# Performance work log

Hardware: AMD Instinct MI355X
Metric: run time of the kernel (lower is better)

## Reference

```python
import jax, jax.numpy as jnp
import numpy as np

N_NODES = 50000
N_EDGES = 600000
D_FEAT = 128
HIDDEN = 128
OUT = 64


def sage_conv(x, src, dst, Wl, bl, Wr, n_nodes):
    # message = x[src] gathered per edge; mean-aggregated at dst
    msg = x[src]                                            # [E, d]
    agg = jax.ops.segment_sum(msg, dst, num_segments=n_nodes)   # [N, d]
    cnt = jax.ops.segment_sum(jnp.ones((src.shape[0],), x.dtype), dst,
                              num_segments=n_nodes)             # [N]
    mean = agg / jnp.maximum(cnt, 1.0)[:, None]
    # PyG SAGEConv: lin_l(mean_neighbors) + lin_r(x_root); only lin_l has bias
    return mean @ Wl + bl + x @ Wr


def setup_inputs() -> dict:
    key = jax.random.key(0)
    ks = jax.random.split(key, 7)
    x = jax.random.normal(ks[0], (N_NODES, D_FEAT), dtype=jnp.float32)
    edge_index = jax.random.randint(ks[1], (2, N_EDGES), 0, N_NODES, dtype=jnp.int64)
    s1 = 1.0 / np.sqrt(D_FEAT)
    s2 = 1.0 / np.sqrt(HIDDEN)
    W1l = jax.random.normal(ks[2], (D_FEAT, HIDDEN), dtype=jnp.float32) * s1
    b1l = jnp.zeros((HIDDEN,), dtype=jnp.float32)
    W1r = jax.random.normal(ks[3], (D_FEAT, HIDDEN), dtype=jnp.float32) * s1
    W2l = jax.random.normal(ks[4], (HIDDEN, OUT), dtype=jnp.float32) * s2
    b2l = jnp.zeros((OUT,), dtype=jnp.float32)
    W2r = jax.random.normal(ks[5], (HIDDEN, OUT), dtype=jnp.float32) * s2
    return {"x": x, "edge_index": edge_index, "W1l": W1l, "b1l": b1l,
            "W1r": W1r, "W2l": W2l, "b2l": b2l, "W2r": W2r}


def reference(x, edge_index, W1l, b1l, W1r, W2l, b2l, W2r):
    n = x.shape[0]
    src, dst = edge_index[0], edge_index[1]
    h = sage_conv(x, src, dst, W1l, b1l, W1r, n)
    h = jax.nn.relu(h)
    out = sage_conv(h, src, dst, W2l, b2l, W2r, n)
    return out
```

## Files before the change

### kernel.cpp

```cpp
#include <hip/hip_runtime.h>
#include <cstdint>
#include <cstddef>

#define D 128
#define O2 64
#define PAD 136
#define CAP 64

typedef __attribute__((ext_vector_type(8))) short bf16x8;
typedef __attribute__((ext_vector_type(4))) float f32x4;

__device__ inline unsigned short f2bf(float f) {
  union { float f; uint32_t u; } v; v.f = f;
  uint32_t r = v.u + 0x7FFF + ((v.u >> 16) & 1);
  return (unsigned short)(r >> 16);
}
__device__ inline float bf_lo(uint32_t w) {
  union { uint32_t u; float f; } v; v.u = w << 16; return v.f;
}
__device__ inline float bf_hi(uint32_t w) {
  union { uint32_t u; float f; } v; v.u = w & 0xFFFF0000u; return v.f;
}

__global__ __launch_bounds__(256) void prep_edges(
    const int* __restrict__ src, const int* __restrict__ dst,
    int* __restrict__ deg, unsigned short* __restrict__ eidx, int n_edges)
{
  const int half = n_edges >> 1;
  int e = blockIdx.x * 256 + threadIdx.x;
  if (e < half) {
    int d0 = dst[e],        d1 = dst[e + half];
    int s0 = src[e],        s1 = src[e + half];
    int p0 = atomicAdd(&deg[d0], 1);
    int p1 = atomicAdd(&deg[d1], 1);
    if (p0 < CAP)
      __builtin_nontemporal_store((unsigned short)s0, eidx + (size_t)d0 * CAP + p0);
    if (p1 < CAP)
      __builtin_nontemporal_store((unsigned short)s1, eidx + (size_t)d1 * CAP + p1);
  }
}

__global__ __launch_bounds__(256) void prep_xw(
    const float* __restrict__ x, const float* __restrict__ W1l,
    const float* __restrict__ W1r, const float* __restrict__ W2l,
    const float* __restrict__ W2r, unsigned short* __restrict__ xb,
    unsigned short* __restrict__ WT1, unsigned short* __restrict__ WT2,
    int n_nodes, int xb_blocks)
{
  int b = blockIdx.x;
  if (b < xb_blocks) {
    int i = b * 256 + threadIdx.x;
    if (i < n_nodes * 32) {
      int n = i >> 5, q = i & 31;
      float4 v = ((const float4*)x)[(size_t)n * 32 + q];
      unsigned long long o =
          (unsigned long long)f2bf(v.x)
        | ((unsigned long long)f2bf(v.y) << 16)
        | ((unsigned long long)f2bf(v.z) << 32)
        | ((unsigned long long)f2bf(v.w) << 48);
      __builtin_nontemporal_store(o, (unsigned long long*)(xb + (size_t)n * 128 + q * 4));
    }
  } else {
    int t = (b - xb_blocks) * 256 + threadIdx.x;
    if (t < 128 * 256) {
      int n = t >> 8, k = t & 255;
      float w = (k < 128) ? W1l[(size_t)k * 128 + n] : W1r[(size_t)(k - 128) * 128 + n];
      WT1[t] = f2bf(w);
    } else {
      int u = t - 128 * 256;
      if (u < 128 * 128) {
        int n = u >> 7, k = u & 127;
        float w = (n < 64) ? W2l[(size_t)k * 64 + n] : W2r[(size_t)k * 64 + (n - 64)];
        WT2[u] = f2bf(w);
      }
    }
  }
}

__global__ __launch_bounds__(256) void gather1_kernel(
    const unsigned short* __restrict__ xb, const unsigned short* __restrict__ eidx,
    const int* __restrict__ deg, unsigned short* __restrict__ mean, int n_nodes)
{
  const int j = threadIdx.x & 7;
  const int g = threadIdx.x >> 3;
  const int n = blockIdx.x * 32 + g;
  if (n >= n_nodes) return;
  const int dg = deg[n];
  const int cnt = min(dg, CAP);
  const unsigned short* bucket = eidx + (size_t)n * CAP;
  float a[16];
  #pragma unroll
  for (int i = 0; i < 16; i++) a[i] = 0.f;
  int p = 0;
  for (; p + 8 <= cnt; p += 8) {
    uint4 bi = *(const uint4*)(bucket + p);
    int s[8];
    s[0] = bi.x & 0xFFFF; s[1] = bi.x >> 16;
    s[2] = bi.y & 0xFFFF; s[3] = bi.y >> 16;
    s[4] = bi.z & 0xFFFF; s[5] = bi.z >> 16;
    s[6] = bi.w & 0xFFFF; s[7] = bi.w >> 16;
    uint4 v0[8], v1[8];
    #pragma unroll
    for (int q = 0; q < 8; q++) {
      const unsigned short* r = xb + (size_t)s[q] * 128 + j * 16;
      v0[q] = *(const uint4*)r;
      v1[q] = *(const uint4*)(r + 8);
    }
    #pragma unroll
    for (int q = 0; q < 8; q++) {
      a[0]+=bf_lo(v0[q].x); a[1]+=bf_hi(v0[q].x);
      a[2]+=bf_lo(v0[q].y); a[3]+=bf_hi(v0[q].y);
      a[4]+=bf_lo(v0[q].z); a[5]+=bf_hi(v0[q].z);
      a[6]+=bf_lo(v0[q].w); a[7]+=bf_hi(v0[q].w);
      a[8]+=bf_lo(v1[q].x); a[9]+=bf_hi(v1[q].x);
      a[10]+=bf_lo(v1[q].y); a[11]+=bf_hi(v1[q].y);
      a[12]+=bf_lo(v1[q].z); a[13]+=bf_hi(v1[q].z);
      a[14]+=bf_lo(v1[q].w); a[15]+=bf_hi(v1[q].w);
    }
  }
  for (; p + 4 <= cnt; p += 4) {
    uint2 bi = *(const uint2*)(bucket + p);
    int s[4];
    s[0] = bi.x & 0xFFFF; s[1] = bi.x >> 16;
    s[2] = bi.y & 0xFFFF; s[3] = bi.y >> 16;
    uint4 v0[4], v1[4];
    #pragma unroll
    for (int q = 0; q < 4; q++) {
      const unsigned short* r = xb + (size_t)s[q] * 128 + j * 16;
      v0[q] = *(const uint4*)r;
      v1[q] = *(const uint4*)(r + 8);
    }
    #pragma unroll
    for (int q = 0; q < 4; q++) {
      a[0]+=bf_lo(v0[q].x); a[1]+=bf_hi(v0[q].x);
      a[2]+=bf_lo(v0[q].y); a[3]+=bf_hi(v0[q].y);
      a[4]+=bf_lo(v0[q].z); a[5]+=bf_hi(v0[q].z);
      a[6]+=bf_lo(v0[q].w); a[7]+=bf_hi(v0[q].w);
      a[8]+=bf_lo(v1[q].x); a[9]+=bf_hi(v1[q].x);
      a[10]+=bf_lo(v1[q].y); a[11]+=bf_hi(v1[q].y);
      a[12]+=bf_lo(v1[q].z); a[13]+=bf_hi(v1[q].z);
      a[14]+=bf_lo(v1[q].w); a[15]+=bf_hi(v1[q].w);
    }
  }
  for (; p < cnt; p++) {
    const unsigned short* rA = xb + (size_t)bucket[p] * 128 + j * 16;
    uint4 vA0 = *(const uint4*)rA, vA1 = *(const uint4*)(rA + 8);
    a[0]+=bf_lo(vA0.x); a[1]+=bf_hi(vA0.x); a[2]+=bf_lo(vA0.y); a[3]+=bf_hi(vA0.y);
    a[4]+=bf_lo(vA0.z); a[5]+=bf_hi(vA0.z); a[6]+=bf_lo(vA0.w); a[7]+=bf_hi(vA0.w);
    a[8]+=bf_lo(vA1.x); a[9]+=bf_hi(vA1.x); a[10]+=bf_lo(vA1.y); a[11]+=bf_hi(vA1.y);
    a[12]+=bf_lo(vA1.z); a[13]+=bf_hi(vA1.z); a[14]+=bf_lo(vA1.w); a[15]+=bf_hi(vA1.w);
  }
  const float ic = 1.0f / fmaxf((float)dg, 1.0f);
  uint4 o0, o1;
  o0.x = ((uint32_t)f2bf(a[1]*ic) << 16) | f2bf(a[0]*ic);
  o0.y = ((uint32_t)f2bf(a[3]*ic) << 16) | f2bf(a[2]*ic);
  o0.z = ((uint32_t)f2bf(a[5]*ic) << 16) | f2bf(a[4]*ic);
  o0.w = ((uint32_t)f2bf(a[7]*ic) << 16) | f2bf(a[6]*ic);
  o1.x = ((uint32_t)f2bf(a[9]*ic) << 16) | f2bf(a[8]*ic);
  o1.y = ((uint32_t)f2bf(a[11]*ic) << 16) | f2bf(a[10]*ic);
  o1.z = ((uint32_t)f2bf(a[13]*ic) << 16) | f2bf(a[12]*ic);
  o1.w = ((uint32_t)f2bf(a[15]*ic) << 16) | f2bf(a[14]*ic);
  unsigned short* mr = mean + (size_t)n * 128 + j * 16;
  *(uint4*)mr = o0;
  *(uint4*)(mr + 8) = o1;
}

__global__ __launch_bounds__(64, 2) void l12_mfma(
    const unsigned short* __restrict__ mean, const unsigned short* __restrict__ xb,
    const unsigned short* __restrict__ WT1, const unsigned short* __restrict__ WT2,
    const float* __restrict__ b1l, unsigned short* __restrict__ hl,
    float* __restrict__ outp, int n_nodes)
{
  __shared__ unsigned short s_h[32 * PAD];
  const int lane = threadIdx.x;
  const int quad = lane >> 4, l15 = lane & 15;
  const int N0 = blockIdx.x * 32;
  const int ra0 = min(N0 + l15, n_nodes - 1);
  const int ra1 = min(N0 + 16 + l15, n_nodes - 1);

  bf16x8 af[2][8];
  #pragma unroll
  for (int s = 0; s < 4; s++) {
    af[0][s]     = *(const bf16x8*)(mean + (size_t)ra0 * 128 + quad * 8 + s * 32);
    af[1][s]     = *(const bf16x8*)(mean + (size_t)ra1 * 128 + quad * 8 + s * 32);
    af[0][s + 4] = *(const bf16x8*)(xb   + (size_t)ra0 * 128 + quad * 8 + s * 32);
    af[1][s + 4] = *(const bf16x8*)(xb   + (size_t)ra1 * 128 + quad * 8 + s * 32);
  }

  f32x4 acc[2][8];
  #pragma unroll
  for (int rt = 0; rt < 2; rt++)
    #pragma unroll
    for (int tt = 0; tt < 8; tt++) acc[rt][tt] = (f32x4){0.f, 0.f, 0.f, 0.f};

  const unsigned short* b1 = WT1 + (size_t)l15 * 256 + quad * 8;
  bf16x8 cur[8], nxt[8];
  #pragma unroll
  for (int s = 0; s < 8; s++) cur[s] = *(const bf16x8*)(b1 + s * 32);
  #pragma unroll
  for (int tt = 0; tt < 8; tt++) {
    if (tt < 7) {
      #pragma unroll
      for (int s = 0; s < 8; s++)
        nxt[s] = *(const bf16x8*)(b1 + (size_t)(tt + 1) * 16 * 256 + s * 32);
    }
    #pragma unroll
    for (int s = 0; s < 8; s++) {
      acc[0][tt] = __builtin_amdgcn_mfma_f32_16x16x32_bf16(af[0][s], cur[s], acc[0][tt], 0, 0, 0);
      acc[1][tt] = __builtin_amdgcn_mfma_f32_16x16x32_bf16(af[1][s], cur[s], acc[1][tt], 0, 0, 0);
    }
    #pragma unroll
    for (int s = 0; s < 8; s++) cur[s] = nxt[s];
  }

  #pragma unroll
  for (int tt = 0; tt < 8; tt++) {
    int col = tt * 16 + l15;
    float bias = b1l[col];
    #pragma unroll
    for (int rt = 0; rt < 2; rt++) {
      int rb = rt * 16 + quad * 4;
      #pragma unroll
      for (int r = 0; r < 4; r++)
        s_h[(rb + r) * PAD + col] = f2bf(fmaxf(acc[rt][tt][r] + bias, 0.f));
    }
  }
  __syncthreads();

  bf16x8 af2[2][4];
  #pragma unroll
  for (int s = 0; s < 4; s++) {
    af2[0][s] = *(const bf16x8*)(s_h + (l15)      * PAD + quad * 8 + s * 32);
    af2[1][s] = *(const bf16x8*)(s_h + (16 + l15) * PAD + quad * 8 + s * 32);
  }
  f32x4 acc2[2][8];
  #pragma unroll
  for (int rt = 0; rt < 2; rt++)
    #pragma unroll
    for (int tt = 0; tt < 8; tt++) acc2[rt][tt] = (f32x4){0.f, 0.f, 0.f, 0.f};

  const unsigned short* b2 = WT2 + (size_t)l15 * 128 + quad * 8;
  bf16x8 cur2[4], nxt2[4];
  #pragma unroll
  for (int s = 0; s < 4; s++) cur2[s] = *(const bf16x8*)(b2 + s * 32);
  #pragma unroll
  for (int tt = 0; tt < 8; tt++) {
    if (tt < 7) {
      #pragma unroll
      for (int s = 0; s < 4; s++)
        nxt2[s] = *(const bf16x8*)(b2 + (size_t)(tt + 1) * 16 * 128 + s * 32);
    }
    #pragma unroll
    for (int s = 0; s < 4; s++) {
      acc2[0][tt] = __builtin_amdgcn_mfma_f32_16x16x32_bf16(af2[0][s], cur2[s], acc2[0][tt], 0, 0, 0);
      acc2[1][tt] = __builtin_amdgcn_mfma_f32_16x16x32_bf16(af2[1][s], cur2[s], acc2[1][tt], 0, 0, 0);
    }
    #pragma unroll
    for (int s = 0; s < 4; s++) cur2[s] = nxt2[s];
  }

  #pragma unroll
  for (int tt = 0; tt < 8; tt++) {
    int col = tt * 16 + l15;
    #pragma unroll
    for (int rt = 0; rt < 2; rt++) {
      int rowb = N0 + rt * 16 + quad * 4;
      #pragma unroll
      for (int r = 0; r < 4; r++) {
        int row = rowb + r;
        if (row < n_nodes) {
          if (tt < 4) hl[(size_t)row * 64 + col] = f2bf(acc2[rt][tt][r]);
          else        outp[(size_t)row * 64 + (col - 64)] = acc2[rt][tt][r];
        }
      }
    }
  }
}

__global__ __launch_bounds__(256) void gather2_kernel(
    const unsigned short* __restrict__ hl, const unsigned short* __restrict__ eidx,
    const int* __restrict__ deg, const float* __restrict__ b2l,
    float* __restrict__ out, int n_nodes)
{
  const int j = threadIdx.x & 7;
  const int g = threadIdx.x >> 3;
  const int n = blockIdx.x * 32 + g;
  if (n >= n_nodes) return;
  const int dg = deg[n];
  const int cnt = min(dg, CAP);
  const unsigned short* bucket = eidx + (size_t)n * CAP;
  float a[8];
  #pragma unroll
  for (int i = 0; i < 8; i++) a[i] = 0.f;
  int p = 0;
  for (; p + 8 <= cnt; p += 8) {
    uint4 bi = *(const uint4*)(bucket + p);
    int s[8];
    s[0] = bi.x & 0xFFFF; s[1] = bi.x >> 16;
    s[2] = bi.y & 0xFFFF; s[3] = bi.y >> 16;
    s[4] = bi.z & 0xFFFF; s[5] = bi.z >> 16;
    s[6] = bi.w & 0xFFFF; s[7] = bi.w >> 16;
    uint4 v[8];
    #pragma unroll
    for (int q = 0; q < 8; q++)
      v[q] = *(const uint4*)(hl + (size_t)s[q] * 64 + j * 8);
    #pragma unroll
    for (int q = 0; q < 8; q++) {
      a[0]+=bf_lo(v[q].x); a[1]+=bf_hi(v[q].x);
      a[2]+=bf_lo(v[q].y); a[3]+=bf_hi(v[q].y);
      a[4]+=bf_lo(v[q].z); a[5]+=bf_hi(v[q].z);
      a[6]+=bf_lo(v[q].w); a[7]+=bf_hi(v[q].w);
    }
  }
  for (; p + 4 <= cnt; p += 4) {
    uint2 bi = *(const uint2*)(bucket + p);
    int s[4];
    s[0] = bi.x & 0xFFFF; s[1] = bi.x >> 16;
    s[2] = bi.y & 0xFFFF; s[3] = bi.y >> 16;
    uint4 v[4];
    #pragma unroll
    for (int q = 0; q < 4; q++)
      v[q] = *(const uint4*)(hl + (size_t)s[q] * 64 + j * 8);
    #pragma unroll
    for (int q = 0; q < 4; q++) {
      a[0]+=bf_lo(v[q].x); a[1]+=bf_hi(v[q].x);
      a[2]+=bf_lo(v[q].y); a[3]+=bf_hi(v[q].y);
      a[4]+=bf_lo(v[q].z); a[5]+=bf_hi(v[q].z);
      a[6]+=bf_lo(v[q].w); a[7]+=bf_hi(v[q].w);
    }
  }
  for (; p < cnt; p++) {
    uint4 vA = *(const uint4*)(hl + (size_t)bucket[p] * 64 + j * 8);
    a[0]+=bf_lo(vA.x); a[1]+=bf_hi(vA.x); a[2]+=bf_lo(vA.y); a[3]+=bf_hi(vA.y);
    a[4]+=bf_lo(vA.z); a[5]+=bf_hi(vA.z); a[6]+=bf_lo(vA.w); a[7]+=bf_hi(vA.w);
  }
  const float ic = 1.0f / fmaxf((float)dg, 1.0f);
  float* o = out + (size_t)n * 64 + j * 8;
  const float* bb = b2l + j * 8;
  float4 p0 = *(const float4*)(o);
  float4 p1 = *(const float4*)(o + 4);
  p0.x += bb[0] + a[0] * ic; p0.y += bb[1] + a[1] * ic;
  p0.z += bb[2] + a[2] * ic; p0.w += bb[3] + a[3] * ic;
  p1.x += bb[4] + a[4] * ic; p1.y += bb[5] + a[5] * ic;
  p1.z += bb[6] + a[6] * ic; p1.w += bb[7] + a[7] * ic;
  *(float4*)(o) = p0;
  *(float4*)(o + 4) = p1;
}

extern "C" void kernel_launch(void* const* d_in, const int* in_sizes, int n_in,
                              void* d_out, int out_size, void* d_ws, size_t ws_size,
                              hipStream_t stream)
{
  const float* x   = (const float*)d_in[0];
  const int*   ei  = (const int*)d_in[1];
  const float* W1l = (const float*)d_in[2];
  const float* b1l = (const float*)d_in[3];
  const float* W1r = (const float*)d_in[4];
  const float* W2l = (const float*)d_in[5];
  const float* b2l = (const float*)d_in[6];
  const float* W2r = (const float*)d_in[7];
  float* out = (float*)d_out;

  const int n_nodes = in_sizes[0] / D;
  const int n_edges = in_sizes[1] / 2;
  const int* src = ei;
  const int* dst = ei + n_edges;

  char* ws = (char*)d_ws;
  auto align256 = [](size_t v) { return (v + 255) & ~(size_t)255; };
  const size_t szN = align256((size_t)n_nodes * 4);

  size_t o = 0;
  int* deg = (int*)(ws + o);  o += szN;
  unsigned short* eidx = (unsigned short*)(ws + o); o += align256((size_t)n_nodes * CAP * 2);
  unsigned short* WT1  = (unsigned short*)(ws + o); o += align256(128 * 256 * 2);
  unsigned short* WT2  = (unsigned short*)(ws + o); o += align256(128 * 128 * 2);
  unsigned short* xb   = (unsigned short*)(ws + o); o += align256((size_t)n_nodes * 128 * 2);
  unsigned short* mean = (unsigned short*)(ws + o); o += align256((size_t)n_nodes * 128 * 2);
  unsigned short* hl   = (unsigned short*)(ws + o); o += align256((size_t)n_nodes * 64 * 2);

  hipMemsetAsync(deg, 0, szN, stream);

  const int half = n_edges >> 1;
  const int xb_blocks = (n_nodes * 32 + 255) / 256;
  const int w_blocks  = (128 * 256 + 128 * 128 + 255) / 256;

  prep_edges<<<(half + 255) / 256, 256, 0, stream>>>(src, dst, deg, eidx, n_edges);
  prep_xw<<<xb_blocks + w_blocks, 256, 0, stream>>>(
      x, W1l, W1r, W2l, W2r, xb, WT1, WT2, n_nodes, xb_blocks);

  gather1_kernel<<<(n_nodes + 31) / 32, 256, 0, stream>>>(
      xb, eidx, deg, mean, n_nodes);
  l12_mfma<<<(n_nodes + 31) / 32, 64, 0, stream>>>(
      mean, xb, WT1, WT2, b1l, hl, out, n_nodes);
  gather2_kernel<<<(n_nodes + 31) / 32, 256, 0, stream>>>(
      hl, eidx, deg, b2l, out, n_nodes);
}
```

Measured before the change: 194.3 us.

## Fuse layer-1 gather with MFMA GEMMs and merge prep kernels

Merges the edge-bucketing and feature/weight conversion prep kernels into one launch. Fuses the layer-1 neighbor-mean gather into the MFMA kernel: each 256-thread block gathers 128 nodes' means into shared memory, then four waves each run the two GEMMs on 32 rows. This removes the global mean buffer round trip and two launches. In exchange it uses a 34 KB shared tile per block, which limits occupancy, and the gather and GEMM phases no longer overlap across separate kernels.

After: 194.9 us. About the same (+0.3%).

```diff
diff --git a/kernel.cpp b/kernel.cpp
--- a/kernel.cpp
+++ b/kernel.cpp
@@ -22,34 +22,96 @@
   union { uint32_t u; float f; } v; v.u = w & 0xFFFF0000u; return v.f;
 }
 
-__global__ __launch_bounds__(256) void prep_edges(
+__device__ __forceinline__ void gather16(
+    const unsigned short* __restrict__ xb, const unsigned short* __restrict__ bucket,
+    int cnt, int j, float a[16])
+{
+  int p = 0;
+  for (; p + 8 <= cnt; p += 8) {
+    uint4 bi = *(const uint4*)(bucket + p);
+    int s[8];
+    s[0] = bi.x & 0xFFFF; s[1] = bi.x >> 16;
+    s[2] = bi.y & 0xFFFF; s[3] = bi.y >> 16;
+    s[4] = bi.z & 0xFFFF; s[5] = bi.z >> 16;
+    s[6] = bi.w & 0xFFFF; s[7] = bi.w >> 16;
+    uint4 v0[8], v1[8];
+    #pragma unroll
+    for (int q = 0; q < 8; q++) {
+      const unsigned short* r = xb + (size_t)s[q] * 128 + j * 16;
+      v0[q] = *(const uint4*)r;
+      v1[q] = *(const uint4*)(r + 8);
+    }
+    #pragma unroll
+    for (int q = 0; q < 8; q++) {
+      a[0]+=bf_lo(v0[q].x); a[1]+=bf_hi(v0[q].x);
+      a[2]+=bf_lo(v0[q].y); a[3]+=bf_hi(v0[q].y);
+      a[4]+=bf_lo(v0[q].z); a[5]+=bf_hi(v0[q].z);
+      a[6]+=bf_lo(v0[q].w); a[7]+=bf_hi(v0[q].w);
+      a[8]+=bf_lo(v1[q].x); a[9]+=bf_hi(v1[q].x);
+      a[10]+=bf_lo(v1[q].y); a[11]+=bf_hi(v1[q].y);
+      a[12]+=bf_lo(v1[q].z); a[13]+=bf_hi(v1[q].z);
+      a[14]+=bf_lo(v1[q].w); a[15]+=bf_hi(v1[q].w);
+    }
+  }
+  for (; p + 4 <= cnt; p += 4) {
+    uint2 bi = *(const uint2*)(bucket + p);
+    int s[4];
+    s[0] = bi.x & 0xFFFF; s[1] = bi.x >> 16;
+    s[2] = bi.y & 0xFFFF; s[3] = bi.y >> 16;
+    uint4 v0[4], v1[4];
+    #pragma unroll
+    for (int q = 0; q < 4; q++) {
+      const unsigned short* r = xb + (size_t)s[q] * 128 + j * 16;
+      v0[q] = *(const uint4*)r;
+      v1[q] = *(const uint4*)(r + 8);
+    }
+    #pragma unroll
+    for (int q = 0; q < 4; q++) {
+      a[0]+=bf_lo(v0[q].x); a[1]+=bf_hi(v0[q].x);
+      a[2]+=bf_lo(v0[q].y); a[3]+=bf_hi(v0[q].y);
+      a[4]+=bf_lo(v0[q].z); a[5]+=bf_hi(v0[q].z);
+      a[6]+=bf_lo(v0[q].w); a[7]+=bf_hi(v0[q].w);
+      a[8]+=bf_lo(v1[q].x); a[9]+=bf_hi(v1[q].x);
+      a[10]+=bf_lo(v1[q].y); a[11]+=bf_hi(v1[q].y);
+      a[12]+=bf_lo(v1[q].z); a[13]+=bf_hi(v1[q].z);
+      a[14]+=bf_lo(v1[q].w); a[15]+=bf_hi(v1[q].w);
+    }
+  }
+  for (; p < cnt; p++) {
+    const unsigned short* rA = xb + (size_t)bucket[p] * 128 + j * 16;
+    uint4 vA0 = *(const uint4*)rA, vA1 = *(const uint4*)(rA + 8);
+    a[0]+=bf_lo(vA0.x); a[1]+=bf_hi(vA0.x); a[2]+=bf_lo(vA0.y); a[3]+=bf_hi(vA0.y);
+    a[4]+=bf_lo(vA0.z); a[5]+=bf_hi(vA0.z); a[6]+=bf_lo(vA0.w); a[7]+=bf_hi(vA0.w);
+    a[8]+=bf_lo(vA1.x); a[9]+=bf_hi(vA1.x); a[10]+=bf_lo(vA1.y); a[11]+=bf_hi(vA1.y);
+    a[12]+=bf_lo(vA1.z); a[13]+=bf_hi(vA1.z); a[14]+=bf_lo(vA1.w); a[15]+=bf_hi(vA1.w);
+  }
+}
+
+__global__ __launch_bounds__(256) void prep_all(
     const int* __restrict__ src, const int* __restrict__ dst,
-    int* __restrict__ deg, unsigned short* __restrict__ eidx, int n_edges)
-{
-  const int half = n_edges >> 1;
-  int e = blockIdx.x * 256 + threadIdx.x;
-  if (e < half) {
-    int d0 = dst[e],        d1 = dst[e + half];
-    int s0 = src[e],        s1 = src[e + half];
-    int p0 = atomicAdd(&deg[d0], 1);
-    int p1 = atomicAdd(&deg[d1], 1);
-    if (p0 < CAP)
-      __builtin_nontemporal_store((unsigned short)s0, eidx + (size_t)d0 * CAP + p0);
-    if (p1 < CAP)
-      __builtin_nontemporal_store((unsigned short)s1, eidx + (size_t)d1 * CAP + p1);
-  }
-}
-
-__global__ __launch_bounds__(256) void prep_xw(
+    int* __restrict__ deg, unsigned short* __restrict__ eidx, int n_edges,
     const float* __restrict__ x, const float* __restrict__ W1l,
     const float* __restrict__ W1r, const float* __restrict__ W2l,
     const float* __restrict__ W2r, unsigned short* __restrict__ xb,
     unsigned short* __restrict__ WT1, unsigned short* __restrict__ WT2,
-    int n_nodes, int xb_blocks)
+    int n_nodes, int edge_blocks, int xb_blocks)
 {
   int b = blockIdx.x;
-  if (b < xb_blocks) {
-    int i = b * 256 + threadIdx.x;
+  if (b < edge_blocks) {
+    const int half = n_edges >> 1;
+    int e = b * 256 + threadIdx.x;
+    if (e < half) {
+      int d0 = dst[e],        d1 = dst[e + half];
+      int s0 = src[e],        s1 = src[e + half];
+      int p0 = atomicAdd(&deg[d0], 1);
+      int p1 = atomicAdd(&deg[d1], 1);
+      if (p0 < CAP)
+        __builtin_nontemporal_store((unsigned short)s0, eidx + (size_t)d0 * CAP + p0);
+      if (p1 < CAP)
+        __builtin_nontemporal_store((unsigned short)s1, eidx + (size_t)d1 * CAP + p1);
+    }
+  } else if (b < edge_blocks + xb_blocks) {
+    int i = (b - edge_blocks) * 256 + threadIdx.x;
     if (i < n_nodes * 32) {
       int n = i >> 5, q = i & 31;
       float4 v = ((const float4*)x)[(size_t)n * 32 + q];
@@ -61,7 +123,7 @@
       __builtin_nontemporal_store(o, (unsigned long long*)(xb + (size_t)n * 128 + q * 4));
     }
   } else {
-    int t = (b - xb_blocks) * 256 + threadIdx.x;
+    int t = (b - edge_blocks - xb_blocks) * 256 + threadIdx.x;
     if (t < 128 * 256) {
       int n = t >> 8, k = t & 255;
       float w = (k < 128) ? W1l[(size_t)k * 128 + n] : W1r[(size_t)(k - 128) * 128 + n];
@@ -77,114 +139,65 @@
   }
 }
 
-__global__ __launch_bounds__(256) void gather1_kernel(
+__global__ __launch_bounds__(256, 2) void fused_l12(
     const unsigned short* __restrict__ xb, const unsigned short* __restrict__ eidx,
-    const int* __restrict__ deg, unsigned short* __restrict__ mean, int n_nodes)
+    const int* __restrict__ deg, const unsigned short* __restrict__ WT1,
+    const unsigned short* __restrict__ WT2, const float* __restrict__ b1l,
+    unsigned short* __restrict__ hl, float* __restrict__ outp, int n_nodes)
 {
-  const int j = threadIdx.x & 7;
-  const int g = threadIdx.x >> 3;
-  const int n = blockIdx.x * 32 + g;
-  if (n >= n_nodes) return;
-  const int dg = deg[n];
-  const int cnt = min(dg, CAP);
-  const unsigned short* bucket = eidx + (size_t)n * CAP;
-  float a[16];
-  #pragma unroll
-  for (int i = 0; i < 16; i++) a[i] = 0.f;
-  int p = 0;
-  for (; p + 8 <= cnt; p += 8) {
-    uint4 bi = *(const uint4*)(bucket + p);
-    int s[8];
-    s[0] = bi.x & 0xFFFF; s[1] = bi.x >> 16;
-    s[2] = bi.y & 0xFFFF; s[3] = bi.y >> 16;
-    s[4] = bi.z & 0xFFFF; s[5] = bi.z >> 16;
-    s[6] = bi.w & 0xFFFF; s[7] = bi.w >> 16;
-    uint4 v0[8], v1[8];
-    #pragma unroll
-    for (int q = 0; q < 8; q++) {
-      const unsigned short* r = xb + (size_t)s[q] * 128 + j * 16;
-      v0[q] = *(const uint4*)r;
-      v1[q] = *(const uint4*)(r + 8);
-    }
-    #pragma unroll
-    for (int q = 0; q < 8; q++) {
-      a[0]+=bf_lo(v0[q].x); a[1]+=bf_hi(v0[q].x);
-      a[2]+=bf_lo(v0[q].y); a[3]+=bf_hi(v0[q].y);
-      a[4]+=bf_lo(v0[q].z); a[5]+=bf_hi(v0[q].z);
-      a[6]+=bf_lo(v0[q].w); a[7]+=bf_hi(v0[q].w);
-      a[8]+=bf_lo(v1[q].x); a[9]+=bf_hi(v1[q].x);
-      a[10]+=bf_lo(v1[q].y); a[11]+=bf_hi(v1[q].y);
-      a[12]+=bf_lo(v1[q].z); a[13]+=bf_hi(v1[q].z);
-      a[14]+=bf_lo(v1[q].w); a[15]+=bf_hi(v1[q].w);
-    }
-  }
-  for (; p + 4 <= cnt; p += 4) {
-    uint2 bi = *(const uint2*)(bucket + p);
-    int s[4];
-    s[0] = bi.x & 0xFFFF; s[1] = bi.x >> 16;
-    s[2] = bi.y & 0xFFFF; s[3] = bi.y >> 16;
-    uint4 v0[4], v1[4];
-    #pragma unroll
-    for (int q = 0; q < 4; q++) {
-      const unsigned short* r = xb + (size_t)s[q] * 128 + j * 16;
-      v0[q] = *(const uint4*)r;
-      v1[q] = *(const uint4*)(r + 8);
-    }
-    #pragma unroll
-    for (int q = 0; q < 4; q++) {
-      a[0]+=bf_lo(v0[q].x); a[1]+=bf_hi(v0[q].x);
-      a[2]+=bf_lo(v0[q].y); a[3]+=bf_hi(v0[q].y);
-      a[4]+=bf_lo(v0[q].z); a[5]+=bf_hi(v0[q].z);
-      a[6]+=bf_lo(v0[q].w); a[7]+=bf_hi(v0[q].w);
-      a[8]+=bf_lo(v1[q].x); a[9]+=bf_hi(v1[q].x);
-      a[10]+=bf_lo(v1[q].y); a[11]+=bf_hi(v1[q].y);
-      a[12]+=bf_lo(v1[q].z); a[13]+=bf_hi(v1[q].z);
-      a[14]+=bf_lo(v1[q].w); a[15]+=bf_hi(v1[q].w);
-    }
-  }
-  for (; p < cnt; p++) {
-    const unsigned short* rA = xb + (size_t)bucket[p] * 128 + j * 16;
-    uint4 vA0 = *(const uint4*)rA, vA1 = *(const uint4*)(rA + 8);
-    a[0]+=bf_lo(vA0.x); a[1]+=bf_hi(vA0.x); a[2]+=bf_lo(vA0.y); a[3]+=bf_hi(vA0.y);
-    a[4]+=bf_lo(vA0.z); a[5]+=bf_hi(vA0.z); a[6]+=bf_lo(vA0.w); a[7]+=bf_hi(vA0.w);
-    a[8]+=bf_lo(vA1.x); a[9]+=bf_hi(vA1.x); a[10]+=bf_lo(vA1.y); a[11]+=bf_hi(vA1.y);
-    a[12]+=bf_lo(vA1.z); a[13]+=bf_hi(vA1.z); a[14]+=bf_lo(vA1.w); a[15]+=bf_hi(vA1.w);
-  }
-  const float ic = 1.0f / fmaxf((float)dg, 1.0f);
-  uint4 o0, o1;
-  o0.x = ((uint32_t)f2bf(a[1]*ic) << 16) | f2bf(a[0]*ic);
-  o0.y = ((uint32_t)f2bf(a[3]*ic) << 16) | f2bf(a[2]*ic);
-  o0.z = ((uint32_t)f2bf(a[5]*ic) << 16) | f2bf(a[4]*ic);
-  o0.w = ((uint32_t)f2bf(a[7]*ic) << 16) | f2bf(a[6]*ic);
-  o1.x = ((uint32_t)f2bf(a[9]*ic) << 16) | f2bf(a[8]*ic);
-  o1.y = ((uint32_t)f2bf(a[11]*ic) << 16) | f2bf(a[10]*ic);
-  o1.z = ((uint32_t)f2bf(a[13]*ic) << 16) | f2bf(a[12]*ic);
-  o1.w = ((uint32_t)f2bf(a[15]*ic) << 16) | f2bf(a[14]*ic);
-  unsigned short* mr = mean + (size_t)n * 128 + j * 16;
-  *(uint4*)mr = o0;
-  *(uint4*)(mr + 8) = o1;
-}
-
-__global__ __launch_bounds__(64, 2) void l12_mfma(
-    const unsigned short* __restrict__ mean, const unsigned short* __restrict__ xb,
-    const unsigned short* __restrict__ WT1, const unsigned short* __restrict__ WT2,
-    const float* __restrict__ b1l, unsigned short* __restrict__ hl,
-    float* __restrict__ outp, int n_nodes)
-{
-  __shared__ unsigned short s_h[32 * PAD];
-  const int lane = threadIdx.x;
+  __shared__ unsigned short s_m[128 * PAD];
+  const int NB0 = blockIdx.x * 128;
+
+  {
+    const int j = threadIdx.x & 7;
+    const int g = threadIdx.x >> 3;
+    #pragma unroll 1
+    for (int pass = 0; pass < 4; pass++) {
+      const int nl = pass * 32 + g;
+      const int n = NB0 + nl;
+      float a[16];
+      #pragma unroll
+      for (int i = 0; i < 16; i++) a[i] = 0.f;
+      float ic = 0.f;
+      if (n < n_nodes) {
+        const int dg = deg[n];
+        const int cnt = min(dg, CAP);
+        gather16(xb, eidx + (size_t)n * CAP, cnt, j, a);
+        ic = 1.0f / fmaxf((float)dg, 1.0f);
+      }
+      uint4 o0, o1;
+      o0.x = ((uint32_t)f2bf(a[1]*ic) << 16) | f2bf(a[0]*ic);
+      o0.y = ((uint32_t)f2bf(a[3]*ic) << 16) | f2bf(a[2]*ic);
+      o0.z = ((uint32_t)f2bf(a[5]*ic) << 16) | f2bf(a[4]*ic);
+      o0.w = ((uint32_t)f2bf(a[7]*ic) << 16) | f2bf(a[6]*ic);
+      o1.x = ((uint32_t)f2bf(a[9]*ic) << 16) | f2bf(a[8]*ic);
+      o1.y = ((uint32_t)f2bf(a[11]*ic) << 16) | f2bf(a[10]*ic);
+      o1.z = ((uint32_t)f2bf(a[13]*ic) << 16) | f2bf(a[12]*ic);
+      o1.w = ((uint32_t)f2bf(a[15]*ic) << 16) | f2bf(a[14]*ic);
+      unsigned short* mr = s_m + nl * PAD + j * 16;
+      *(uint4*)mr = o0;
+      *(uint4*)(mr + 8) = o1;
+    }
+  }
+  __syncthreads();
+
+  const int lane = threadIdx.x & 63;
+  const int w    = threadIdx.x >> 6;
   const int quad = lane >> 4, l15 = lane & 15;
-  const int N0 = blockIdx.x * 32;
+  const int N0 = NB0 + w * 32;
   const int ra0 = min(N0 + l15, n_nodes - 1);
   const int ra1 = min(N0 + 16 + l15, n_nodes - 1);
 
+  const unsigned short* sm0 = s_m + (w * 32 + l15) * PAD + quad * 8;
+  const unsigned short* sm1 = sm0 + 16 * PAD;
+
   bf16x8 af[2][8];
   #pragma unroll
   for (int s = 0; s < 4; s++) {
-    af[0][s]     = *(const bf16x8*)(mean + (size_t)ra0 * 128 + quad * 8 + s * 32);
-    af[1][s]     = *(const bf16x8*)(mean + (size_t)ra1 * 128 + quad * 8 + s * 32);
-    af[0][s + 4] = *(const bf16x8*)(xb   + (size_t)ra0 * 128 + quad * 8 + s * 32);
-    af[1][s + 4] = *(const bf16x8*)(xb   + (size_t)ra1 * 128 + quad * 8 + s * 32);
+    af[0][s]     = *(const bf16x8*)(sm0 + s * 32);
+    af[1][s]     = *(const bf16x8*)(sm1 + s * 32);
+    af[0][s + 4] = *(const bf16x8*)(xb + (size_t)ra0 * 128 + quad * 8 + s * 32);
+    af[1][s + 4] = *(const bf16x8*)(xb + (size_t)ra1 * 128 + quad * 8 + s * 32);
   }
 
   f32x4 acc[2][8];
@@ -213,6 +226,7 @@
     for (int s = 0; s < 8; s++) cur[s] = nxt[s];
   }
 
+  unsigned short* s_hw = s_m + (size_t)w * 32 * PAD;
   #pragma unroll
   for (int tt = 0; tt < 8; tt++) {
     int col = tt * 16 + l15;
@@ -222,16 +236,15 @@
       int rb = rt * 16 + quad * 4;
       #pragma unroll
       for (int r = 0; r < 4; r++)
-        s_h[(rb + r) * PAD + col] = f2bf(fmaxf(acc[rt][tt][r] + bias, 0.f));
-    }
-  }
-  __syncthreads();
+        s_hw[(rb + r) * PAD + col] = f2bf(fmaxf(acc[rt][tt][r] + bias, 0.f));
+    }
+  }
 
   bf16x8 af2[2][4];
   #pragma unroll
   for (int s = 0; s < 4; s++) {
-    af2[0][s] = *(const bf16x8*)(s_h + (l15)      * PAD + quad * 8 + s * 32);
-    af2[1][s] = *(const bf16x8*)(s_h + (16 + l15) * PAD + quad * 8 + s * 32);
+    af2[0][s] = *(const bf16x8*)(s_hw + (l15)      * PAD + quad * 8 + s * 32);
+    af2[1][s] = *(const bf16x8*)(s_hw + (16 + l15) * PAD + quad * 8 + s * 32);
   }
   f32x4 acc2[2][8];
   #pragma unroll
@@ -376,23 +389,22 @@
   unsigned short* WT1  = (unsigned short*)(ws + o); o += align256(128 * 256 * 2);
   unsigned short* WT2  = (unsigned short*)(ws + o); o += align256(128 * 128 * 2);
   unsigned short* xb   = (unsigned short*)(ws + o); o += align256((size_t)n_nodes * 128 * 2);
-  unsigned short* mean = (unsigned short*)(ws + o); o += align256((size_t)n_nodes * 128 * 2);
   unsigned short* hl   = (unsigned short*)(ws + o); o += align256((size_t)n_nodes * 64 * 2);
 
   hipMemsetAsync(deg, 0, szN, stream);
 
   const int half = n_edges >> 1;
+  const int edge_blocks = (half + 255) / 256;
   const int xb_blocks = (n_nodes * 32 + 255) / 256;
   const int w_blocks  = (128 * 256 + 128 * 128 + 255) / 256;
 
-  prep_edges<<<(half + 255) / 256, 256, 0, stream>>>(src, dst, deg, eidx, n_edges);
-  prep_xw<<<xb_blocks + w_blocks, 256, 0, stream>>>(
-      x, W1l, W1r, W2l, W2r, xb, WT1, WT2, n_nodes, xb_blocks);
-
-  gather1_kernel<<<(n_nodes + 31) / 32, 256, 0, stream>>>(
-      xb, eidx, deg, mean, n_nodes);
-  l12_mfma<<<(n_nodes + 31) / 32, 64, 0, stream>>>(
-      mean, xb, WT1, WT2, b1l, hl, out, n_nodes);
+  prep_all<<<edge_blocks + xb_blocks + w_blocks, 256, 0, stream>>>(
+      src, dst, deg, eidx, n_edges,
+      x, W1l, W1r, W2l, W2r, xb, WT1, WT2, n_nodes, edge_blocks, xb_blocks);
+
+  fused_l12<<<(n_nodes + 127) / 128, 256, 0, stream>>>(
+      xb, eidx, deg, WT1, WT2, b1l, hl, out, n_nodes);
+
   gather2_kernel<<<(n_nodes + 31) / 32, 256, 0, stream>>>(
       hl, eidx, deg, b2l, out, n_nodes);
 }
```
